# Optimization experiments

Hardware: AMD Instinct MI355X
Metric: run time of the kernel (lower is better)

The kernel has to match this reference:

```python
import jax, jax.numpy as jnp
import numpy as np

NUM_CAPSULE = 10
DIM_CAPSULE = 16
ROUTINGS = 3
EPS = 1e-7  # K.epsilon()


def squash(x, axis=-1):
    # bojone squash: x / sqrt(s2 + eps) * s2 / (1 + s2)
    s2 = jnp.sum(jnp.square(x), axis=axis, keepdims=True)
    return x * s2 / ((1.0 + s2) * jnp.sqrt(s2 + EPS))


def setup_inputs() -> dict:
    key = jax.random.key(0)
    k1, k2 = jax.random.split(key)
    B, N, D_in = 64, 2048, 128  # batch, input_num_capsule, input_dim_capsule
    u_vecs = jax.random.normal(k1, (B, N, D_in), dtype=jnp.float32)
    fan_out = NUM_CAPSULE * DIM_CAPSULE
    limit = float(np.sqrt(6.0 / (D_in + fan_out)))  # glorot_uniform
    W = jax.random.uniform(k2, (D_in, fan_out), dtype=jnp.float32,
                           minval=-limit, maxval=limit)
    return {"u_vecs": u_vecs, "W": W}


def reference(u_vecs, W):
    B, N, _ = u_vecs.shape
    # share_weights=True: conv1d with kernel size 1 == matmul over feature dim
    u_hat = (u_vecs @ W).reshape(B, N, NUM_CAPSULE, DIM_CAPSULE)
    u_hat = jnp.transpose(u_hat, (0, 2, 1, 3))  # (B, J, N, D)
    b = jnp.zeros((B, NUM_CAPSULE, N), dtype=u_vecs.dtype)
    o = jnp.zeros((B, NUM_CAPSULE, DIM_CAPSULE), dtype=u_vecs.dtype)
    for i in range(ROUTINGS):
        c = jax.nn.softmax(b, axis=1)           # softmax over output capsules
        o = jnp.einsum('bjn,bjnd->bjd', c, u_hat)
        if i < ROUTINGS - 1:
            b = jnp.einsum('bjd,bjnd->bjn', o, u_hat)  # agreement update
    return squash(o)
```

## Files before the change

### kernel.cpp

```cpp
#include <hip/hip_runtime.h>
#include <math.h>


#define BATCH 64
#define NN    2048
#define KD    128
#define JCAP  10
#define DCAP  16
#define JDIM  160
#define EPSQ  1e-7f
#define NT    64
#define TROW  32
#define GSTR  132

#define WS_OP 0
#define WS_V  (BATCH * NT * JDIM)

__device__ __forceinline__ void gload16(const float* g, void* l) {
  __builtin_amdgcn_global_load_lds(
      (const __attribute__((address_space(1))) void*)g,
      (__attribute__((address_space(3))) void*)l, 16, 0, 0);
}

__global__ __launch_bounds__(256) void f_iter0(const float* __restrict__ u,
                                               const float* __restrict__ W,
                                               float* __restrict__ Op) {
  const int b = blockIdx.y, tile = blockIdx.x, t = threadIdx.x;
  __shared__ __align__(16) float4 red[256];
  __shared__ float S_s[KD];
  const int c = t & 31, rg = t >> 5;
  const float* p = u + (((size_t)(b * NN + tile * TROW + rg * 4)) << 7) + (c << 2);
  float4 a = make_float4(0.f, 0.f, 0.f, 0.f);
#pragma unroll
  for (int r = 0; r < 4; ++r) {
    const float4 w4 = *(const float4*)(p + ((size_t)r << 7));
    a.x += w4.x; a.y += w4.y; a.z += w4.z; a.w += w4.w;
  }
  red[t] = a;
  __syncthreads();
  if (t < 32) {
    float4 s4 = red[t];
#pragma unroll
    for (int g = 1; g < 8; ++g) {
      const float4 w4 = red[g * 32 + t];
      s4.x += w4.x; s4.y += w4.y; s4.z += w4.z; s4.w += w4.w;
    }
    s4.x *= 0.1f; s4.y *= 0.1f; s4.z *= 0.1f; s4.w *= 0.1f;
    *(float4*)&S_s[t * 4] = s4;
  }
  __syncthreads();
  if (t < JDIM) {
    float acc = 0.f;
#pragma unroll 4
    for (int k = 0; k < KD; ++k) acc += S_s[k] * W[k * JDIM + t];
    Op[((size_t)(b * NT) + tile) * JDIM + t] = acc;
  }
}

__global__ __launch_bounds__(128) void f_makeV(const float* __restrict__ Op,
                                               const float* __restrict__ W,
                                               float* __restrict__ V) {
  const int j = blockIdx.x, b = blockIdx.y, t = threadIdx.x;
  __shared__ float o_s[DCAP];
  if (t < DCAP) {
    float s = 0.f;
    const float* p = Op + (size_t)b * NT * JDIM + j * DCAP + t;
#pragma unroll
    for (int tl = 0; tl < NT; ++tl) s += p[tl * JDIM];
    o_s[t] = s;
  }
  __syncthreads();
  const float* wp = W + t * JDIM + j * DCAP;
  float acc = 0.f;
#pragma unroll
  for (int d = 0; d < DCAP; ++d) acc += wp[d] * o_s[d];
  V[((size_t)(b * JCAP + j) << 7) + t] = acc;
}

__global__ __launch_bounds__(256) void f_route(const float* __restrict__ u,
                                               const float* __restrict__ V,
                                               const float* __restrict__ W,
                                               float* __restrict__ Op) {
  const int b = blockIdx.y, tile = blockIdx.x, t = threadIdx.x;
  const int r0 = tile * TROW;
  __shared__ __align__(16) float4 u4[TROW * 32];
  __shared__ __align__(16) float4 Vs4[JCAP * 32];
  __shared__ __align__(16) float Cs[JCAP][TROW];
  __shared__ __align__(16) float GpPl[JCAP * GSTR];

  {
    const float* ub = u + (((size_t)(b * NN + r0)) << 7);
    const int wbase = t & 192;
#pragma unroll
    for (int p = 0; p < 4; ++p) {
      const int s = p * 256 + t;
      const int r = s >> 5, csl = s & 31;
      const int c = csl ^ (r & 7);
      gload16(ub + (((size_t)r) << 7) + (c << 2), &u4[p * 256 + wbase]);
    }
    const float* vb = V + (((size_t)(b * JCAP)) << 7);
    gload16(vb + (t << 2), &Vs4[wbase]);
    if (t < 64) gload16(vb + ((256 + t) << 2), &Vs4[256]);
  }
  __syncthreads();

  {
    const int r = t & 31, q8 = t >> 5;
    float acc[JCAP];
#pragma unroll
    for (int j = 0; j < JCAP; ++j) acc[j] = 0.f;
#pragma unroll
    for (int c4 = 0; c4 < 4; ++c4) {
      const float4 uu = u4[(r << 5) + ((q8 * 4 + c4) ^ (r & 7))];
#pragma unroll
      for (int j = 0; j < JCAP; ++j) {
        const float4 vv = Vs4[j * 32 + q8 * 4 + c4];
        acc[j] += uu.x * vv.x + uu.y * vv.y + uu.z * vv.z + uu.w * vv.w;
      }
    }
#pragma unroll
    for (int j = 0; j < JCAP; ++j) acc[j] += __shfl_xor(acc[j], 32, 64);
    if ((t & 32) == 0) {
      const int q4 = t >> 6;
#pragma unroll
      for (int j = 0; j < JCAP; ++j) GpPl[(q4 * JCAP + j) * TROW + r] = acc[j];
    }
  }
  __syncthreads();
  if (t < TROW) {
    float lg[JCAP];
    float m = -1e30f;
#pragma unroll
    for (int j = 0; j < JCAP; ++j) {
      const float s = GpPl[j * TROW + t] + GpPl[(JCAP + j) * TROW + t]
                    + GpPl[(2 * JCAP + j) * TROW + t]
                    + GpPl[(3 * JCAP + j) * TROW + t];
      lg[j] = s; m = fmaxf(m, s);
    }
    float ssum = 0.f;
#pragma unroll
    for (int j = 0; j < JCAP; ++j) { lg[j] = __expf(lg[j] - m); ssum += lg[j]; }
    const float inv = 1.f / ssum;
#pragma unroll
    for (int j = 0; j < JCAP; ++j) Cs[j][t] = lg[j] * inv;
  }
  __syncthreads();

  {
    const int w = t >> 6, l = t & 63;
    const int j0 = (w < 2) ? 3 * w : 2 * w + 2;
    const int jn = (w < 2) ? 3 : 2;
    const int chalf = l >> 1, cin = (l & 1) << 1;
    float g0[3], g1[3];
#pragma unroll
    for (int jj = 0; jj < 3; ++jj) { g0[jj] = 0.f; g1[jj] = 0.f; }
    for (int rc = 0; rc < TROW; rc += 4) {
      float ua[4], uc[4];
#pragma unroll
      for (int qq = 0; qq < 4; ++qq) {
        const int r = rc + qq;
        const float2 uu2 =
            *(const float2*)((const float*)&u4[(r << 5) + (chalf ^ (r & 7))] + cin);
        ua[qq] = uu2.x; uc[qq] = uu2.y;
      }
#pragma unroll
      for (int jj = 0; jj < 3; ++jj) {
        if (jj < jn) {
          const float4 c4v = *(const float4*)&Cs[j0 + jj][rc];
          g0[jj] += c4v.x * ua[0] + c4v.y * ua[1] + c4v.z * ua[2] + c4v.w * ua[3];
          g1[jj] += c4v.x * uc[0] + c4v.y * uc[1] + c4v.z * uc[2] + c4v.w * uc[3];
        }
      }
    }
#pragma unroll
    for (int jj = 0; jj < 3; ++jj)
      if (jj < jn)
        *(float2*)&GpPl[(j0 + jj) * GSTR + 2 * l] = make_float2(g0[jj], g1[jj]);
  }
  __syncthreads();
  if (t < JDIM) {
    const int j = t >> 4;
    const float* gj = GpPl + j * GSTR;
    float acc = 0.f;
#pragma unroll 4
    for (int k = 0; k < KD; ++k) acc += gj[k] * W[k * JDIM + t];
    Op[((size_t)(b * NT) + tile) * JDIM + t] = acc;
  }
}

__global__ __launch_bounds__(192) void f_squash(const float* __restrict__ Op,
                                                float* __restrict__ out) {
  const int b = blockIdx.x, t = threadIdx.x;
  __shared__ float o_s[JDIM];
  __shared__ float sc[JCAP];
  if (t < JDIM) {
    float s = 0.f;
    const float* p = Op + (size_t)b * NT * JDIM + t;
#pragma unroll
    for (int tl = 0; tl < NT; ++tl) s += p[tl * JDIM];
    o_s[t] = s;
  }
  __syncthreads();
  if (t < JCAP) {
    float s2 = 0.f;
#pragma unroll
    for (int d = 0; d < DCAP; ++d) { const float x = o_s[t * DCAP + d]; s2 += x * x; }
    sc[t] = s2 / ((1.f + s2) * sqrtf(s2 + EPSQ));
  }
  __syncthreads();
  if (t < JDIM) out[b * JDIM + t] = o_s[t] * sc[t >> 4];
}

extern "C" void kernel_launch(void* const* d_in, const int* in_sizes, int n_in,
                              void* d_out, int out_size, void* d_ws, size_t ws_size,
                              hipStream_t stream) {
  const float* u = (const float*)d_in[0];
  const float* W = (const float*)d_in[1];
  float* out = (float*)d_out;
  float* ws  = (float*)d_ws;

  float* Op = ws + WS_OP;
  float* V  = ws + WS_V;
  f_iter0 <<<dim3(NT, BATCH), 256, 0, stream>>>(u, W, Op);
  f_makeV <<<dim3(JCAP, BATCH), 128, 0, stream>>>(Op, W, V);
  f_route <<<dim3(NT, BATCH), 256, 0, stream>>>(u, V, W, Op);
  f_makeV <<<dim3(JCAP, BATCH), 128, 0, stream>>>(Op, W, V);
  f_route <<<dim3(NT, BATCH), 256, 0, stream>>>(u, V, W, Op);
  f_squash<<<BATCH, 192, 0, stream>>>(Op, out);
}
```

Baseline: 180.9 us.

## Double rows per routing tile, read V via scalar loads, reduce logits with LDS atomics

Raises the rows per tile from 32 to 64 and halves the tile count, so the per-tile W projection and the Op partial sums are amortised over more rows. The route kernel no longer stages V in LDS. Each wave instead holds its row's u chunk in registers and reads V through wave-uniform (readfirstlane) addresses, so those loads can become scalar loads. Per-wave partial logits are combined with LDS atomicAdd rather than shuffles and per-quarter buffers. The cost is fewer blocks (2048 instead of 4096), more LDS per block and more register pressure, which may lower occupancy.

```diff
diff --git a/kernel.cpp b/kernel.cpp
--- a/kernel.cpp
+++ b/kernel.cpp
@@ -9,8 +9,8 @@
 #define DCAP  16
 #define JDIM  160
 #define EPSQ  1e-7f
-#define NT    64
-#define TROW  32
+#define NT    32
+#define TROW  64
 #define GSTR  132
 
 #define WS_OP 0
@@ -29,10 +29,10 @@
   __shared__ __align__(16) float4 red[256];
   __shared__ float S_s[KD];
   const int c = t & 31, rg = t >> 5;
-  const float* p = u + (((size_t)(b * NN + tile * TROW + rg * 4)) << 7) + (c << 2);
+  const float* p = u + (((size_t)(b * NN + tile * TROW + rg * 8)) << 7) + (c << 2);
   float4 a = make_float4(0.f, 0.f, 0.f, 0.f);
 #pragma unroll
-  for (int r = 0; r < 4; ++r) {
+  for (int r = 0; r < 8; ++r) {
     const float4 w4 = *(const float4*)(p + ((size_t)r << 7));
     a.x += w4.x; a.y += w4.y; a.z += w4.z; a.w += w4.w;
   }
@@ -84,7 +84,6 @@
   const int b = blockIdx.y, tile = blockIdx.x, t = threadIdx.x;
   const int r0 = tile * TROW;
   __shared__ __align__(16) float4 u4[TROW * 32];
-  __shared__ __align__(16) float4 Vs4[JCAP * 32];
   __shared__ __align__(16) float Cs[JCAP][TROW];
   __shared__ __align__(16) float GpPl[JCAP * GSTR];
 
@@ -92,39 +91,39 @@
     const float* ub = u + (((size_t)(b * NN + r0)) << 7);
     const int wbase = t & 192;
 #pragma unroll
-    for (int p = 0; p < 4; ++p) {
+    for (int p = 0; p < 8; ++p) {
       const int s = p * 256 + t;
       const int r = s >> 5, csl = s & 31;
       const int c = csl ^ (r & 7);
       gload16(ub + (((size_t)r) << 7) + (c << 2), &u4[p * 256 + wbase]);
     }
-    const float* vb = V + (((size_t)(b * JCAP)) << 7);
-    gload16(vb + (t << 2), &Vs4[wbase]);
-    if (t < 64) gload16(vb + ((256 + t) << 2), &Vs4[256]);
-  }
+  }
+  for (int i = t; i < JCAP * TROW; i += 256) GpPl[i] = 0.f;
   __syncthreads();
 
   {
-    const int r = t & 31, q8 = t >> 5;
+    const int r = t & 63, rx = r & 7;
+    const int q = __builtin_amdgcn_readfirstlane(t >> 6);
+    const int ubase = (r << 5) + (q << 3);
+    float4 ur[8];
+#pragma unroll
+    for (int c = 0; c < 8; ++c) ur[c] = u4[ubase + (c ^ rx)];
+    const int voff = __builtin_amdgcn_readfirstlane(b * JCAP * KD + (q << 5));
+    const float* vp = V + voff;
     float acc[JCAP];
 #pragma unroll
-    for (int j = 0; j < JCAP; ++j) acc[j] = 0.f;
-#pragma unroll
-    for (int c4 = 0; c4 < 4; ++c4) {
-      const float4 uu = u4[(r << 5) + ((q8 * 4 + c4) ^ (r & 7))];
-#pragma unroll
-      for (int j = 0; j < JCAP; ++j) {
-        const float4 vv = Vs4[j * 32 + q8 * 4 + c4];
-        acc[j] += uu.x * vv.x + uu.y * vv.y + uu.z * vv.z + uu.w * vv.w;
+    for (int j = 0; j < JCAP; ++j) {
+      const float* vj = vp + (j << 7);
+      float a = 0.f;
+#pragma unroll
+      for (int c = 0; c < 8; ++c) {
+        const float4 vv = *(const float4*)(vj + (c << 2));
+        a += ur[c].x * vv.x + ur[c].y * vv.y + ur[c].z * vv.z + ur[c].w * vv.w;
       }
-    }
-#pragma unroll
-    for (int j = 0; j < JCAP; ++j) acc[j] += __shfl_xor(acc[j], 32, 64);
-    if ((t & 32) == 0) {
-      const int q4 = t >> 6;
-#pragma unroll
-      for (int j = 0; j < JCAP; ++j) GpPl[(q4 * JCAP + j) * TROW + r] = acc[j];
-    }
+      acc[j] = a;
+    }
+#pragma unroll
+    for (int j = 0; j < JCAP; ++j) atomicAdd(&GpPl[j * TROW + r], acc[j]);
   }
   __syncthreads();
   if (t < TROW) {
@@ -132,15 +131,12 @@
     float m = -1e30f;
 #pragma unroll
     for (int j = 0; j < JCAP; ++j) {
-      const float s = GpPl[j * TROW + t] + GpPl[(JCAP + j) * TROW + t]
-                    + GpPl[(2 * JCAP + j) * TROW + t]
-                    + GpPl[(3 * JCAP + j) * TROW + t];
-      lg[j] = s; m = fmaxf(m, s);
-    }
-    float ssum = 0.f;
-#pragma unroll
-    for (int j = 0; j < JCAP; ++j) { lg[j] = __expf(lg[j] - m); ssum += lg[j]; }
-    const float inv = 1.f / ssum;
+      lg[j] = GpPl[j * TROW + t]; m = fmaxf(m, lg[j]);
+    }
+    float ss = 0.f;
+#pragma unroll
+    for (int j = 0; j < JCAP; ++j) { lg[j] = __expf(lg[j] - m); ss += lg[j]; }
+    const float inv = 1.f / ss;
 #pragma unroll
     for (int j = 0; j < JCAP; ++j) Cs[j][t] = lg[j] * inv;
   }
@@ -154,21 +150,25 @@
     float g0[3], g1[3];
 #pragma unroll
     for (int jj = 0; jj < 3; ++jj) { g0[jj] = 0.f; g1[jj] = 0.f; }
-    for (int rc = 0; rc < TROW; rc += 4) {
-      float ua[4], uc[4];
-#pragma unroll
-      for (int qq = 0; qq < 4; ++qq) {
-        const int r = rc + qq;
+#pragma unroll
+    for (int o = 0; o < 8; ++o) {
+      float ua[8], uc[8];
+#pragma unroll
+      for (int ri = 0; ri < 8; ++ri) {
+        const int r = o * 8 + ri;
         const float2 uu2 =
-            *(const float2*)((const float*)&u4[(r << 5) + (chalf ^ (r & 7))] + cin);
-        ua[qq] = uu2.x; uc[qq] = uu2.y;
+            *(const float2*)((const float*)&u4[(r << 5) + (chalf ^ ri)] + cin);
+        ua[ri] = uu2.x; uc[ri] = uu2.y;
       }
 #pragma unroll
       for (int jj = 0; jj < 3; ++jj) {
         if (jj < jn) {
-          const float4 c4v = *(const float4*)&Cs[j0 + jj][rc];
-          g0[jj] += c4v.x * ua[0] + c4v.y * ua[1] + c4v.z * ua[2] + c4v.w * ua[3];
-          g1[jj] += c4v.x * uc[0] + c4v.y * uc[1] + c4v.z * uc[2] + c4v.w * uc[3];
+          const float4 cA = *(const float4*)&Cs[j0 + jj][o * 8];
+          const float4 cB = *(const float4*)&Cs[j0 + jj][o * 8 + 4];
+          g0[jj] += cA.x * ua[0] + cA.y * ua[1] + cA.z * ua[2] + cA.w * ua[3]
+                  + cB.x * ua[4] + cB.y * ua[5] + cB.z * ua[6] + cB.w * ua[7];
+          g1[jj] += cA.x * uc[0] + cA.y * uc[1] + cA.z * uc[2] + cA.w * uc[3]
+                  + cB.x * uc[4] + cB.y * uc[5] + cB.z * uc[6] + cB.w * uc[7];
         }
       }
     }
@@ -182,7 +182,7 @@
     const int j = t >> 4;
     const float* gj = GpPl + j * GSTR;
     float acc = 0.f;
-#pragma unroll 4
+#pragma unroll 8
     for (int k = 0; k < KD; ++k) acc += gj[k] * W[k * JDIM + t];
     Op[((size_t)(b * NT) + tile) * JDIM + t] = acc;
   }
```

Measured after the change: 220.8 us. 22.0% more time.

## Defer W projection out of per-tile route kernels into per-batch fold kernel

Applied to the files above, without the earlier changes.

The per-tile projections through W in f_iter0 and f_route are removed. Each tile now writes its raw 128-dim weighted sums (10x128 per tile) to workspace, and a new f_fold kernel reduces across tiles first, then applies W once per batch/capsule. Squash is merged into the last fold pass. This removes the serial 128-step W matvec from every tile block, at the cost of writing and reading an 8x larger partial buffer. The softmax scratch is also merged into the partial-sum buffer and the C·u loop is unrolled more.

```diff
diff --git a/kernel.cpp b/kernel.cpp
--- a/kernel.cpp
+++ b/kernel.cpp
@@ -11,10 +11,9 @@
 #define EPSQ  1e-7f
 #define NT    64
 #define TROW  32
-#define GSTR  132
-
-#define WS_OP 0
-#define WS_V  (BATCH * NT * JDIM)
+
+#define WS_GP 0
+#define WS_V  (BATCH * NT * JCAP * KD)
 
 __device__ __forceinline__ void gload16(const float* g, void* l) {
   __builtin_amdgcn_global_load_lds(
@@ -23,11 +22,9 @@
 }
 
 __global__ __launch_bounds__(256) void f_iter0(const float* __restrict__ u,
-                                               const float* __restrict__ W,
-                                               float* __restrict__ Op) {
+                                               float* __restrict__ Sp) {
   const int b = blockIdx.y, tile = blockIdx.x, t = threadIdx.x;
   __shared__ __align__(16) float4 red[256];
-  __shared__ float S_s[KD];
   const int c = t & 31, rg = t >> 5;
   const float* p = u + (((size_t)(b * NN + tile * TROW + rg * 4)) << 7) + (c << 2);
   float4 a = make_float4(0.f, 0.f, 0.f, 0.f);
@@ -45,48 +42,60 @@
       const float4 w4 = red[g * 32 + t];
       s4.x += w4.x; s4.y += w4.y; s4.z += w4.z; s4.w += w4.w;
     }
-    s4.x *= 0.1f; s4.y *= 0.1f; s4.z *= 0.1f; s4.w *= 0.1f;
-    *(float4*)&S_s[t * 4] = s4;
-  }
-  __syncthreads();
-  if (t < JDIM) {
-    float acc = 0.f;
-#pragma unroll 4
-    for (int k = 0; k < KD; ++k) acc += S_s[k] * W[k * JDIM + t];
-    Op[((size_t)(b * NT) + tile) * JDIM + t] = acc;
-  }
-}
-
-__global__ __launch_bounds__(128) void f_makeV(const float* __restrict__ Op,
-                                               const float* __restrict__ W,
-                                               float* __restrict__ V) {
+    *(float4*)&Sp[(size_t)(b * NT + tile) * KD + t * 4] = s4;
+  }
+}
+
+__global__ __launch_bounds__(128) void f_fold(const float* __restrict__ In,
+                                              const float* __restrict__ W,
+                                              float* __restrict__ Out, int pass) {
   const int j = blockIdx.x, b = blockIdx.y, t = threadIdx.x;
+  __shared__ float g_s[KD];
   __shared__ float o_s[DCAP];
+  if (pass == 0) {
+    const float* p = In + (size_t)b * NT * KD + t;
+    float s = 0.f;
+#pragma unroll 8
+    for (int tl = 0; tl < NT; ++tl) s += p[(size_t)tl * KD];
+    g_s[t] = s * 0.1f;
+  } else {
+    const float* p = In + ((size_t)(b * NT) * JCAP + j) * KD + t;
+    float s = 0.f;
+#pragma unroll 8
+    for (int tl = 0; tl < NT; ++tl) s += p[(size_t)tl * JCAP * KD];
+    g_s[t] = s;
+  }
+  __syncthreads();
   if (t < DCAP) {
-    float s = 0.f;
-    const float* p = Op + (size_t)b * NT * JDIM + j * DCAP + t;
-#pragma unroll
-    for (int tl = 0; tl < NT; ++tl) s += p[tl * JDIM];
-    o_s[t] = s;
-  }
-  __syncthreads();
-  const float* wp = W + t * JDIM + j * DCAP;
-  float acc = 0.f;
-#pragma unroll
-  for (int d = 0; d < DCAP; ++d) acc += wp[d] * o_s[d];
-  V[((size_t)(b * JCAP + j) << 7) + t] = acc;
+    float a = 0.f;
+#pragma unroll 8
+    for (int k = 0; k < KD; ++k) a += g_s[k] * W[k * JDIM + j * DCAP + t];
+    o_s[t] = a;
+  }
+  __syncthreads();
+  if (pass < 2) {
+    const float* wp = W + t * JDIM + j * DCAP;
+    float a = 0.f;
+#pragma unroll
+    for (int d = 0; d < DCAP; ++d) a += wp[d] * o_s[d];
+    Out[((size_t)(b * JCAP) + j) * KD + t] = a;
+  } else if (t < DCAP) {
+    float s2 = 0.f;
+#pragma unroll
+    for (int d = 0; d < DCAP; ++d) s2 += o_s[d] * o_s[d];
+    const float sc = s2 / ((1.f + s2) * sqrtf(s2 + EPSQ));
+    Out[(size_t)(b * JCAP + j) * DCAP + t] = o_s[t] * sc;
+  }
 }
 
 __global__ __launch_bounds__(256) void f_route(const float* __restrict__ u,
                                                const float* __restrict__ V,
-                                               const float* __restrict__ W,
-                                               float* __restrict__ Op) {
+                                               float* __restrict__ Gp) {
   const int b = blockIdx.y, tile = blockIdx.x, t = threadIdx.x;
   const int r0 = tile * TROW;
   __shared__ __align__(16) float4 u4[TROW * 32];
   __shared__ __align__(16) float4 Vs4[JCAP * 32];
-  __shared__ __align__(16) float Cs[JCAP][TROW];
-  __shared__ __align__(16) float GpPl[JCAP * GSTR];
+  __shared__ __align__(16) float PlCs[4 * JCAP * TROW];
 
   {
     const float* ub = u + (((size_t)(b * NN + r0)) << 7);
@@ -123,7 +132,7 @@
     if ((t & 32) == 0) {
       const int q4 = t >> 6;
 #pragma unroll
-      for (int j = 0; j < JCAP; ++j) GpPl[(q4 * JCAP + j) * TROW + r] = acc[j];
+      for (int j = 0; j < JCAP; ++j) PlCs[(q4 * JCAP + j) * TROW + r] = acc[j];
     }
   }
   __syncthreads();
@@ -132,17 +141,17 @@
     float m = -1e30f;
 #pragma unroll
     for (int j = 0; j < JCAP; ++j) {
-      const float s = GpPl[j * TROW + t] + GpPl[(JCAP + j) * TROW + t]
-                    + GpPl[(2 * JCAP + j) * TROW + t]
-                    + GpPl[(3 * JCAP + j) * TROW + t];
+      const float s = PlCs[j * TROW + t] + PlCs[(JCAP + j) * TROW + t]
+                    + PlCs[(2 * JCAP + j) * TROW + t]
+                    + PlCs[(3 * JCAP + j) * TROW + t];
       lg[j] = s; m = fmaxf(m, s);
     }
-    float ssum = 0.f;
-#pragma unroll
-    for (int j = 0; j < JCAP; ++j) { lg[j] = __expf(lg[j] - m); ssum += lg[j]; }
-    const float inv = 1.f / ssum;
-#pragma unroll
-    for (int j = 0; j < JCAP; ++j) Cs[j][t] = lg[j] * inv;
+    float ss = 0.f;
+#pragma unroll
+    for (int j = 0; j < JCAP; ++j) { lg[j] = __expf(lg[j] - m); ss += lg[j]; }
+    const float inv = 1.f / ss;
+#pragma unroll
+    for (int j = 0; j < JCAP; ++j) PlCs[j * TROW + t] = lg[j] * inv;
   }
   __syncthreads();
 
@@ -154,61 +163,34 @@
     float g0[3], g1[3];
 #pragma unroll
     for (int jj = 0; jj < 3; ++jj) { g0[jj] = 0.f; g1[jj] = 0.f; }
-    for (int rc = 0; rc < TROW; rc += 4) {
-      float ua[4], uc[4];
-#pragma unroll
-      for (int qq = 0; qq < 4; ++qq) {
-        const int r = rc + qq;
+#pragma unroll
+    for (int o = 0; o < 4; ++o) {
+      float ua[8], uc[8];
+#pragma unroll
+      for (int ri = 0; ri < 8; ++ri) {
+        const int r = o * 8 + ri;
         const float2 uu2 =
-            *(const float2*)((const float*)&u4[(r << 5) + (chalf ^ (r & 7))] + cin);
-        ua[qq] = uu2.x; uc[qq] = uu2.y;
+            *(const float2*)((const float*)&u4[(r << 5) + (chalf ^ ri)] + cin);
+        ua[ri] = uu2.x; uc[ri] = uu2.y;
       }
 #pragma unroll
       for (int jj = 0; jj < 3; ++jj) {
         if (jj < jn) {
-          const float4 c4v = *(const float4*)&Cs[j0 + jj][rc];
-          g0[jj] += c4v.x * ua[0] + c4v.y * ua[1] + c4v.z * ua[2] + c4v.w * ua[3];
-          g1[jj] += c4v.x * uc[0] + c4v.y * uc[1] + c4v.z * uc[2] + c4v.w * uc[3];
+          const float4 cA = *(const float4*)&PlCs[(j0 + jj) * TROW + o * 8];
+          const float4 cB = *(const float4*)&PlCs[(j0 + jj) * TROW + o * 8 + 4];
+          g0[jj] += cA.x * ua[0] + cA.y * ua[1] + cA.z * ua[2] + cA.w * ua[3]
+                  + cB.x * ua[4] + cB.y * ua[5] + cB.z * ua[6] + cB.w * ua[7];
+          g1[jj] += cA.x * uc[0] + cA.y * uc[1] + cA.z * uc[2] + cA.w * uc[3]
+                  + cB.x * uc[4] + cB.y * uc[5] + cB.z * uc[6] + cB.w * uc[7];
         }
       }
     }
+    float* gb = Gp + ((size_t)(b * NT + tile)) * JCAP * KD;
 #pragma unroll
     for (int jj = 0; jj < 3; ++jj)
       if (jj < jn)
-        *(float2*)&GpPl[(j0 + jj) * GSTR + 2 * l] = make_float2(g0[jj], g1[jj]);
-  }
-  __syncthreads();
-  if (t < JDIM) {
-    const int j = t >> 4;
-    const float* gj = GpPl + j * GSTR;
-    float acc = 0.f;
-#pragma unroll 4
-    for (int k = 0; k < KD; ++k) acc += gj[k] * W[k * JDIM + t];
-    Op[((size_t)(b * NT) + tile) * JDIM + t] = acc;
-  }
-}
-
-__global__ __launch_bounds__(192) void f_squash(const float* __restrict__ Op,
-                                                float* __restrict__ out) {
-  const int b = blockIdx.x, t = threadIdx.x;
-  __shared__ float o_s[JDIM];
-  __shared__ float sc[JCAP];
-  if (t < JDIM) {
-    float s = 0.f;
-    const float* p = Op + (size_t)b * NT * JDIM + t;
-#pragma unroll
-    for (int tl = 0; tl < NT; ++tl) s += p[tl * JDIM];
-    o_s[t] = s;
-  }
-  __syncthreads();
-  if (t < JCAP) {
-    float s2 = 0.f;
-#pragma unroll
-    for (int d = 0; d < DCAP; ++d) { const float x = o_s[t * DCAP + d]; s2 += x * x; }
-    sc[t] = s2 / ((1.f + s2) * sqrtf(s2 + EPSQ));
-  }
-  __syncthreads();
-  if (t < JDIM) out[b * JDIM + t] = o_s[t] * sc[t >> 4];
+        *(float2*)&gb[(j0 + jj) * KD + 2 * l] = make_float2(g0[jj], g1[jj]);
+  }
 }
 
 extern "C" void kernel_launch(void* const* d_in, const int* in_sizes, int n_in,
@@ -219,12 +201,12 @@
   float* out = (float*)d_out;
   float* ws  = (float*)d_ws;
 
-  float* Op = ws + WS_OP;
+  float* Gp = ws + WS_GP;
   float* V  = ws + WS_V;
-  f_iter0 <<<dim3(NT, BATCH), 256, 0, stream>>>(u, W, Op);
-  f_makeV <<<dim3(JCAP, BATCH), 128, 0, stream>>>(Op, W, V);
-  f_route <<<dim3(NT, BATCH), 256, 0, stream>>>(u, V, W, Op);
-  f_makeV <<<dim3(JCAP, BATCH), 128, 0, stream>>>(Op, W, V);
-  f_route <<<dim3(NT, BATCH), 256, 0, stream>>>(u, V, W, Op);
-  f_squash<<<BATCH, 192, 0, stream>>>(Op, out);
-}
+  f_iter0 <<<dim3(NT, BATCH), 256, 0, stream>>>(u, Gp);
+  f_fold  <<<dim3(JCAP, BATCH), 128, 0, stream>>>(Gp, W, V, 0);
+  f_route <<<dim3(NT, BATCH), 256, 0, stream>>>(u, V, Gp);
+  f_fold  <<<dim3(JCAP, BATCH), 128, 0, stream>>>(Gp, W, V, 1);
+  f_route <<<dim3(NT, BATCH), 256, 0, stream>>>(u, V, Gp);
+  f_fold  <<<dim3(JCAP, BATCH), 128, 0, stream>>>(Gp, W, out, 2);
+}
```

Result: faster. 168.7 us (-6.8%).
